# Kernel tuning notes

Measured on AMD Instinct MI355X. Metric: run time of the kernel, lower is better.

The kernel has to match this reference:

```python
import jax, jax.numpy as jnp
from jax import lax
import numpy as np

B, CIN, CP, H, W = 16, 64, 64, 64, 64
K1 = 3   # deformable kernel
K2 = 5   # parallel conv kernel
EPS = 1e-5


def conv2d(x, w, stride, pad):
    return lax.conv_general_dilated(
        x, w, (stride, stride), [(pad, pad), (pad, pad)],
        dimension_numbers=('NCHW', 'OIHW', 'NCHW'))


def batchnorm(x, g, b, m, v):
    scale = g / jnp.sqrt(v + EPS)
    return (x - m[None, :, None, None]) * scale[None, :, None, None] + b[None, :, None, None]


def deform_conv2d(x, offset, weight, stride, pad):
    # x: [B,Cin,H,W], offset: [B,2*K*K,Ho,Wo] (dy,dx interleaved per kernel tap, torchvision layout)
    Bn, Cin, Hn, Wn = x.shape
    Cout, _, K, _ = weight.shape
    KK = K * K
    Ho, Wo = offset.shape[2], offset.shape[3]
    off = offset.reshape(Bn, KK, 2, Ho, Wo)
    dy, dx = off[:, :, 0], off[:, :, 1]                      # [B,KK,Ho,Wo]
    ky, kx = jnp.meshgrid(jnp.arange(K), jnp.arange(K), indexing='ij')
    ky = ky.reshape(KK).astype(x.dtype)
    kx = kx.reshape(KK).astype(x.dtype)
    base_y = (jnp.arange(Ho) * stride - pad).astype(x.dtype)
    base_x = (jnp.arange(Wo) * stride - pad).astype(x.dtype)
    ys = base_y[None, None, :, None] + ky[None, :, None, None] + dy  # [B,KK,Ho,Wo]
    xs = base_x[None, None, None, :] + kx[None, :, None, None] + dx
    y0 = jnp.floor(ys); x0 = jnp.floor(xs)
    wy1 = ys - y0; wx1 = xs - x0
    wy0 = 1.0 - wy1; wx0 = 1.0 - wx1
    flat = x.reshape(Bn, Cin, Hn * Wn)

    def gather(yi, xi):
        valid = ((yi >= 0) & (yi <= Hn - 1) & (xi >= 0) & (xi <= Wn - 1))
        yc = jnp.clip(yi, 0, Hn - 1).astype(jnp.int32)
        xc = jnp.clip(xi, 0, Wn - 1).astype(jnp.int32)
        idx = (yc * Wn + xc).reshape(Bn, -1)                 # [B,KK*Ho*Wo]
        g = jax.vmap(lambda f, i: jnp.take(f, i, axis=1))(flat, idx)
        g = g.reshape(Bn, Cin, KK, Ho, Wo)
        return g * valid.astype(x.dtype)[:, None]

    val = (gather(y0, x0) * (wy0 * wx0)[:, None]
           + gather(y0, x0 + 1) * (wy0 * wx1)[:, None]
           + gather(y0 + 1, x0) * (wy1 * wx0)[:, None]
           + gather(y0 + 1, x0 + 1) * (wy1 * wx1)[:, None])   # [B,Cin,KK,Ho,Wo]
    w_r = weight.reshape(Cout, Cin, KK)
    return jnp.einsum('bcknm,ock->bonm', val, w_r)


def setup_inputs():
    key = jax.random.key(0)
    ks = jax.random.split(key, 18)
    f32 = jnp.float32
    x = jax.random.normal(ks[0], (B, CIN, H, W), f32)
    w_off = jax.random.normal(ks[1], (2 * K1 * K1, CIN, 3, 3), f32) * 0.01
    b_off = jnp.zeros((2 * K1 * K1,), f32)
    w1 = jax.random.normal(ks[2], (CP, CIN, K1, K1), f32) / np.sqrt(CIN * K1 * K1)
    w3 = jax.random.normal(ks[3], (CP, CIN, K2, K2), f32) / np.sqrt(CIN * K2 * K2)
    w2 = jax.random.normal(ks[4], (CP, CP, 3, 3), f32) / np.sqrt(CP * 9)
    def bn(i):
        g = jax.random.uniform(ks[5 + 4 * i], (CP,), f32, 0.5, 1.5)
        b = jax.random.normal(ks[6 + 4 * i], (CP,), f32) * 0.1
        m = jax.random.normal(ks[7 + 4 * i], (CP,), f32) * 0.1
        v = jax.random.uniform(ks[8 + 4 * i], (CP,), f32, 0.5, 1.5)
        return g, b, m, v
    g1, b1, m1, v1 = bn(0)
    g3, b3, m3, v3 = bn(1)
    g2, b2, m2, v2 = bn(2)
    return dict(x=x, w_off=w_off, b_off=b_off, w1=w1, g1=g1, b1=b1, m1=m1, v1=v1,
                w3=w3, g3=g3, b3=b3, m3=m3, v3=v3, w2=w2, g2=g2, b2=b2, m2=m2, v2=v2)


def reference(x, w_off, b_off, w1, g1, b1, m1, v1, w3, g3, b3, m3, v3, w2, g2, b2, m2, v2):
    offset1 = conv2d(x, w_off, 1, 1) + b_off[None, :, None, None]
    out = jax.nn.relu(batchnorm(deform_conv2d(x, offset1, w1, 1, 1), g1, b1, m1, v1))
    out_1 = jax.nn.relu(batchnorm(conv2d(x, w3, 1, 2), g3, b3, m3, v3))
    out = out + out_1
    out = batchnorm(conv2d(out, w2, 1, 1), g2, b2, m2, v2)
    out = out + x  # identity shortcut (stride=1, in_planes==planes)
    return jax.nn.relu(out)
```

## Files before the change

kernel.cpp:

```cpp
#include <hip/hip_runtime.h>
#include <hip/hip_bf16.h>


#define HWv 4096
#define EPSv 1e-5f

typedef __attribute__((ext_vector_type(8))) short bf16x8;
typedef __attribute__((ext_vector_type(16))) float f32x16;
typedef __attribute__((ext_vector_type(2))) float f32x2;

__device__ inline ushort f2bf(float f) {
  __hip_bfloat16 h = __float2bfloat16(f);
  return *(ushort*)&h;
}
__device__ inline float bitsf(unsigned int u) {
  union { unsigned int i; float f; } c; c.i = u; return c.f;
}

__global__ __launch_bounds__(256) void prep_kernel(
    const float* __restrict__ x, const float* __restrict__ w3,
    const float* __restrict__ w2, const float* __restrict__ w1,
    const float* __restrict__ w_off,
    ushort* __restrict__ xT, ushort* __restrict__ w3F,
    ushort* __restrict__ w2F, ushort* __restrict__ w1F,
    ushort* __restrict__ wofF) {
  __shared__ float tile[64][65];
  const int blk = blockIdx.x;
  if (blk < 1024) {
    const int y = blk & 63, b = blk >> 6;
    for (int i = threadIdx.x; i < 4096; i += 256) {
      int ci = i >> 6, xx = i & 63;
      tile[ci][xx] = x[(((size_t)b * 64 + ci) * 64 + y) * 64 + xx];
    }
    __syncthreads();
    for (int i = threadIdx.x; i < 2048; i += 256) {
      int xx = i >> 5, cip = (i & 31) * 2;
      ushort2 v;
      v.x = f2bf(tile[cip][xx]);
      v.y = f2bf(tile[cip + 1][xx]);
      *(ushort2*)&xT[(((size_t)b * 64 + y) * 64 + xx) * 64 + cip] = v;
    }
    return;
  }
  int idx = (blk - 1024) * 256 + threadIdx.x;
  if (idx < 102400) {
    int j = idx & 7, lane = (idx >> 3) & 63, ks = (idx >> 9) & 3;
    int half = (idx >> 11) & 1, kk = idx >> 12;
    int ln = lane & 31, kh = lane >> 5;
    int co = half * 32 + ln, ci = ks * 16 + kh * 8 + j;
    w3F[idx] = f2bf(w3[(co * 64 + ci) * 25 + kk]);
    return;
  }
  idx -= 102400;
  if (idx < 36864) {
    int j = idx & 7, lane = (idx >> 3) & 63, ks = (idx >> 9) & 3;
    int half = (idx >> 11) & 1, kk = idx >> 12;
    int ln = lane & 31, kh = lane >> 5;
    int co = half * 32 + ln, ci = ks * 16 + kh * 8 + j;
    w2F[idx] = f2bf(w2[(co * 64 + ci) * 9 + kk]);
    return;
  }
  idx -= 36864;
  if (idx < 36864) {
    int j = idx & 7, lane = (idx >> 3) & 63, ks = (idx >> 9) & 3;
    int half = (idx >> 11) & 1, kk = idx >> 12;
    int ln = lane & 31, kh = lane >> 5;
    int co = half * 32 + ln, ci = ks * 16 + kh * 8 + j;
    w1F[idx] = f2bf(w1[(co * 64 + ci) * 9 + kk]);
    return;
  }
  idx -= 36864;
  if (idx < 18432) {
    int j = idx & 7, lane = (idx >> 3) & 63, ks = (idx >> 9) & 3;
    int kk = idx >> 11;
    int ln = lane & 31, kh = lane >> 5;
    int ci = ks * 16 + kh * 8 + j;
    wofF[idx] = f2bf(ln < 18 ? w_off[(ln * 64 + ci) * 9 + kk] : 0.f);
  }
}

__device__ __forceinline__ bf16x8 blend4(bf16x8 va, bf16x8 vb, bf16x8 vc, bf16x8 vd,
                                         f32x2 w00v, f32x2 w01v, f32x2 w10v, f32x2 w11v) {
  const unsigned int* ua = (const unsigned int*)&va;
  const unsigned int* ub = (const unsigned int*)&vb;
  const unsigned int* uc = (const unsigned int*)&vc;
  const unsigned int* ud = (const unsigned int*)&vd;
  bf16x8 f;
  ushort2* fo = (ushort2*)&f;
#pragma unroll
  for (int d = 0; d < 4; ++d) {
    f32x2 av = {bitsf(ua[d] << 16), bitsf(ua[d] & 0xFFFF0000u)};
    f32x2 bv = {bitsf(ub[d] << 16), bitsf(ub[d] & 0xFFFF0000u)};
    f32x2 cv = {bitsf(uc[d] << 16), bitsf(uc[d] & 0xFFFF0000u)};
    f32x2 dv = {bitsf(ud[d] << 16), bitsf(ud[d] & 0xFFFF0000u)};
    f32x2 r = w00v * av + w01v * bv + w10v * cv + w11v * dv;
    __hip_bfloat162 h2 = __float22bfloat162_rn(make_float2(r.x, r.y));
    fo[d] = *(ushort2*)&h2;
  }
  return f;
}

__global__ __launch_bounds__(512, 4) void fused_kernel(
    const ushort* __restrict__ xT, const ushort* __restrict__ wofF,
    const float* __restrict__ b_off, const ushort* __restrict__ w1F,
    const ushort* __restrict__ w3F,
    const float* __restrict__ g1, const float* __restrict__ b1,
    const float* __restrict__ m1, const float* __restrict__ v1,
    const float* __restrict__ g3, const float* __restrict__ b3,
    const float* __restrict__ m3, const float* __restrict__ v3,
    ushort* __restrict__ s1T) {
  __shared__ __align__(16) unsigned char smem[71680];
  uint4* ldsx = (uint4*)smem;
  float* stash = (float*)(smem + 52224);
  float* bn1s = (float*)(smem + 70656);
  float* bn1b = bn1s + 64;
  float* bn3s = bn1s + 128;
  float* bn3b = bn1s + 192;

  const int tid = threadIdx.x;
  const int wv = tid >> 6, lane = tid & 63;
  const int ln = lane & 31, kh = lane >> 5;
  const int role = wv & 1, nt = (wv >> 1) & 1, r = wv >> 2;
  const int y0 = blockIdx.x * 2, b = blockIdx.y;
  const int y = y0 + r, px = nt * 32 + ln;
  const uint4* xT4 = (const uint4*)xT;
  const bool interior = (y0 >= 2 && y0 <= 60);

  if (tid < 64) {
    float s = g1[tid] * rsqrtf(v1[tid] + EPSv);
    bn1s[tid] = s; bn1b[tid] = b1[tid] - m1[tid] * s;
    float s3 = g3[tid] * rsqrtf(v3[tid] + EPSv);
    bn3s[tid] = s3; bn3b[tid] = b3[tid] - m3[tid] * s3;
  }
  for (int i = tid; i < 6 * 68 * 8; i += 512) {
    int tr = i / (68 * 8), rem = i % (68 * 8);
    int col = rem >> 3, c = rem & 7;
    int ysrc = min(max(y0 - 2 + tr, 0), 63);
    int xcol = col - 2;
    uint4 v = make_uint4(0, 0, 0, 0);
    if (xcol >= 0 && xcol <= 63)
      v = xT4[((size_t)((b * 64 + ysrc) * 64 + xcol)) * 8 + c];
    ldsx[(tr * 68 + col) * 8 + (c ^ (col & 7))] = v;
  }
  __syncthreads();

  {
    f32x16 acco;
#pragma unroll
    for (int j = 0; j < 16; ++j) acco[j] = 0.f;
    if (interior) {
#pragma unroll
      for (int kk = 0; kk < 9; ++kk) {
        const int ky = kk / 3, kx = kk % 3;
        const int tr = r + ky + 1;
        const int col = px + kx + 1;
#pragma unroll
        for (int ksq = 0; ksq < 2; ++ksq) {
          int ks = role * 2 + ksq;
          int c = ks * 2 + kh;
          bf16x8 af = *(const bf16x8*)&wofF[(size_t)((kk * 4 + ks) * 64 + lane) * 8];
          bf16x8 bf = *(const bf16x8*)&ldsx[(tr * 68 + col) * 8 + (c ^ (col & 7))];
          acco = __builtin_amdgcn_mfma_f32_32x32x16_bf16(af, bf, acco, 0, 0, 0);
        }
      }
    } else {
#pragma unroll
      for (int kk = 0; kk < 9; ++kk) {
        const int ky = kk / 3, kx = kk % 3;
        const int yy = y - 1 + ky;
        if (yy >= 0 && yy <= 63) {
          const int tr = yy - (y0 - 2);
          const int col = px + kx + 1;
#pragma unroll
          for (int ksq = 0; ksq < 2; ++ksq) {
            int ks = role * 2 + ksq;
            int c = ks * 2 + kh;
            bf16x8 af = *(const bf16x8*)&wofF[(size_t)((kk * 4 + ks) * 64 + lane) * 8];
            bf16x8 bf = *(const bf16x8*)&ldsx[(tr * 68 + col) * 8 + (c ^ (col & 7))];
            acco = __builtin_amdgcn_mfma_f32_32x32x16_bf16(af, bf, acco, 0, 0, 0);
          }
        }
      }
    }
    float* stb = stash + role * 2304;
#pragma unroll
    for (int reg = 0; reg < 16; ++reg) {
      int co = (reg & 3) + 8 * (reg >> 2) + 4 * kh;
      if (co < 18)
        stb[(r * 64 + px) * 18 + co] = acco[reg] + (role ? 0.f : b_off[co]);
    }
  }
  __syncthreads();

  f32x16 accA, accB;
#pragma unroll
  for (int j = 0; j < 16; ++j) { accA[j] = 0.f; accB[j] = 0.f; }

  if (role == 0) {
    float dyv[9], dxv[9];
    const int sb = (r * 64 + px) * 18;
#pragma unroll
    for (int kk = 0; kk < 9; ++kk) {
      dyv[kk] = stash[sb + 2 * kk] + stash[2304 + sb + 2 * kk];
      dxv[kk] = stash[sb + 2 * kk + 1] + stash[2304 + sb + 2 * kk + 1];
    }
    bool fast = true;
#pragma unroll
    for (int kk = 0; kk < 9; ++kk) {
      int iy0 = (int)floorf((float)(y - 1 + kk / 3) + dyv[kk]);
      int iy1 = iy0 + 1;
      bool ok0 = (iy0 < 0) || (iy0 > 63) || (iy0 >= y0 - 2 && iy0 <= y0 + 3);
      bool ok1 = (iy1 < 0) || (iy1 > 63) || (iy1 >= y0 - 2 && iy1 <= y0 + 3);
      fast = fast && ok0 && ok1;
    }
    const ushort* xb = xT + (size_t)b * 64 * 64 * 64;

    if (__ballot(!fast) == 0ull) {
#pragma unroll
      for (int kk = 0; kk < 9; ++kk) {
        const int ky = kk / 3, kx = kk % 3;
        float ys = (float)(y - 1 + ky) + dyv[kk];
        float xs = (float)(px - 1 + kx) + dxv[kk];
        float y0f = floorf(ys), x0f = floorf(xs);
        float wy1 = ys - y0f, wx1 = xs - x0f;
        float wy0 = 1.f - wy1, wx0 = 1.f - wx1;
        int iy0 = (int)y0f, ix0 = (int)x0f;
        int iy1 = iy0 + 1, ix1 = ix0 + 1;
        float vy0 = (iy0 >= 0 && iy0 <= 63) ? 1.f : 0.f;
        float vy1 = (iy1 >= 0 && iy1 <= 63) ? 1.f : 0.f;
        float vx0 = (ix0 >= 0 && ix0 <= 63) ? 1.f : 0.f;
        float vx1 = (ix1 >= 0 && ix1 <= 63) ? 1.f : 0.f;
        int x0c = min(max(ix0, 0), 63), x1c = min(max(ix1, 0), 63);
        float w00 = wy0 * wx0 * vy0 * vx0;
        float w01 = wy0 * wx1 * vy0 * vx1;
        float w10 = wy1 * wx0 * vy1 * vx0;
        float w11 = wy1 * wx1 * vy1 * vx1;
        int tr0 = min(max(iy0 - (y0 - 2), 0), 5);
        int tr1 = min(max(iy1 - (y0 - 2), 0), 5);
        int c0 = x0c + 2, c1 = x1c + 2;
        f32x2 w00v = {w00, w00}, w01v = {w01, w01};
        f32x2 w10v = {w10, w10}, w11v = {w11, w11};
#pragma unroll
        for (int ks = 0; ks < 4; ++ks) {
          int c = ks * 2 + kh;
          bf16x8 va = *(const bf16x8*)&ldsx[(tr0 * 68 + c0) * 8 + (c ^ (c0 & 7))];
          bf16x8 vb = *(const bf16x8*)&ldsx[(tr0 * 68 + c1) * 8 + (c ^ (c1 & 7))];
          bf16x8 vc = *(const bf16x8*)&ldsx[(tr1 * 68 + c0) * 8 + (c ^ (c0 & 7))];
          bf16x8 vd = *(const bf16x8*)&ldsx[(tr1 * 68 + c1) * 8 + (c ^ (c1 & 7))];
          bf16x8 f = blend4(va, vb, vc, vd, w00v, w01v, w10v, w11v);
          bf16x8 a0 = *(const bf16x8*)&w1F[(size_t)(((kk * 2 + 0) * 4 + ks) * 64 + lane) * 8];
          bf16x8 a1 = *(const bf16x8*)&w1F[(size_t)(((kk * 2 + 1) * 4 + ks) * 64 + lane) * 8];
          accA = __builtin_amdgcn_mfma_f32_32x32x16_bf16(a0, f, accA, 0, 0, 0);
          accB = __builtin_amdgcn_mfma_f32_32x32x16_bf16(a1, f, accB, 0, 0, 0);
        }
      }
    } else {
#pragma unroll
      for (int kk = 0; kk < 9; ++kk) {
        const int ky = kk / 3, kx = kk % 3;
        float ys = (float)(y - 1 + ky) + dyv[kk];
        float xs = (float)(px - 1 + kx) + dxv[kk];
        float y0f = floorf(ys), x0f = floorf(xs);
        float wy1 = ys - y0f, wx1 = xs - x0f;
        float wy0 = 1.f - wy1, wx0 = 1.f - wx1;
        int iy0 = (int)y0f, ix0 = (int)x0f;
        int iy1 = iy0 + 1, ix1 = ix0 + 1;
        float vy0 = (iy0 >= 0 && iy0 <= 63) ? 1.f : 0.f;
        float vy1 = (iy1 >= 0 && iy1 <= 63) ? 1.f : 0.f;
        float vx0 = (ix0 >= 0 && ix0 <= 63) ? 1.f : 0.f;
        float vx1 = (ix1 >= 0 && ix1 <= 63) ? 1.f : 0.f;
        int x0c = min(max(ix0, 0), 63), x1c = min(max(ix1, 0), 63);
        float w00 = wy0 * wx0 * vy0 * vx0;
        float w01 = wy0 * wx1 * vy0 * vx1;
        float w10 = wy1 * wx0 * vy1 * vx0;
        float w11 = wy1 * wx1 * vy1 * vx1;
        int tr0 = min(max(iy0 - (y0 - 2), 0), 5);
        int tr1 = min(max(iy1 - (y0 - 2), 0), 5);
        int c0 = x0c + 2, c1 = x1c + 2;
        f32x2 w00v = {w00, w00}, w01v = {w01, w01};
        f32x2 w10v = {w10, w10}, w11v = {w11, w11};
        int y0c = min(max(iy0, 0), 63), y1c = min(max(iy1, 0), 63);
        const ushort* p00 = xb + (y0c * 64 + x0c) * 64 + kh * 8;
        const ushort* p01 = xb + (y0c * 64 + x1c) * 64 + kh * 8;
        const ushort* p10 = xb + (y1c * 64 + x0c) * 64 + kh * 8;
        const ushort* p11 = xb + (y1c * 64 + x1c) * 64 + kh * 8;
#pragma unroll
        for (int ks = 0; ks < 4; ++ks) {
          int c = ks * 2 + kh;
          bf16x8 va = *(const bf16x8*)&ldsx[(tr0 * 68 + c0) * 8 + (c ^ (c0 & 7))];
          bf16x8 vb = *(const bf16x8*)&ldsx[(tr0 * 68 + c1) * 8 + (c ^ (c1 & 7))];
          bf16x8 vc = *(const bf16x8*)&ldsx[(tr1 * 68 + c0) * 8 + (c ^ (c0 & 7))];
          bf16x8 vd = *(const bf16x8*)&ldsx[(tr1 * 68 + c1) * 8 + (c ^ (c1 & 7))];
          bf16x8 f = blend4(va, vb, vc, vd, w00v, w01v, w10v, w11v);
          if (!fast) {
            bf16x8 ga = *(const bf16x8*)(p00 + ks * 16);
            bf16x8 gb = *(const bf16x8*)(p01 + ks * 16);
            bf16x8 gc = *(const bf16x8*)(p10 + ks * 16);
            bf16x8 gd = *(const bf16x8*)(p11 + ks * 16);
            f = blend4(ga, gb, gc, gd, w00v, w01v, w10v, w11v);
          }
          bf16x8 a0 = *(const bf16x8*)&w1F[(size_t)(((kk * 2 + 0) * 4 + ks) * 64 + lane) * 8];
          bf16x8 a1 = *(const bf16x8*)&w1F[(size_t)(((kk * 2 + 1) * 4 + ks) * 64 + lane) * 8];
          accA = __builtin_amdgcn_mfma_f32_32x32x16_bf16(a0, f, accA, 0, 0, 0);
          accB = __builtin_amdgcn_mfma_f32_32x32x16_bf16(a1, f, accB, 0, 0, 0);
        }
      }
    }
  } else {
    if (interior) {
#pragma unroll
      for (int kk = 0; kk < 25; ++kk) {
        const int ky = kk / 5, kx = kk % 5;
        const int tr = r + ky;
        const int col = px + kx;
        bf16x8 a0[4], a1[4], bfv[4];
#pragma unroll
        for (int ks = 0; ks < 4; ++ks) {
          a0[ks] = *(const bf16x8*)&w3F[(size_t)(((kk * 2 + 0) * 4 + ks) * 64 + lane) * 8];
          a1[ks] = *(const bf16x8*)&w3F[(size_t)(((kk * 2 + 1) * 4 + ks) * 64 + lane) * 8];
        }
#pragma unroll
        for (int ks = 0; ks < 4; ++ks) {
          int c = ks * 2 + kh;
          bfv[ks] = *(const bf16x8*)&ldsx[(tr * 68 + col) * 8 + (c ^ (col & 7))];
        }
#pragma unroll
        for (int ks = 0; ks < 4; ++ks) {
          accA = __builtin_amdgcn_mfma_f32_32x32x16_bf16(a0[ks], bfv[ks], accA, 0, 0, 0);
          accB = __builtin_amdgcn_mfma_f32_32x32x16_bf16(a1[ks], bfv[ks], accB, 0, 0, 0);
        }
      }
    } else {
#pragma unroll
      for (int kk = 0; kk < 25; ++kk) {
        const int ky = kk / 5, kx = kk % 5;
        const int yy = y - 2 + ky;
        if (yy >= 0 && yy <= 63) {
          const int tr = r + ky;
          const int col = px + kx;
#pragma unroll
          for (int ks = 0; ks < 4; ++ks) {
            int c = ks * 2 + kh;
            bf16x8 bf = *(const bf16x8*)&ldsx[(tr * 68 + col) * 8 + (c ^ (col & 7))];
            bf16x8 a0 = *(const bf16x8*)&w3F[(size_t)(((kk * 2 + 0) * 4 + ks) * 64 + lane) * 8];
            bf16x8 a1 = *(const bf16x8*)&w3F[(size_t)(((kk * 2 + 1) * 4 + ks) * 64 + lane) * 8];
            accA = __builtin_amdgcn_mfma_f32_32x32x16_bf16(a0, bf, accA, 0, 0, 0);
            accB = __builtin_amdgcn_mfma_f32_32x32x16_bf16(a1, bf, accB, 0, 0, 0);
          }
        }
      }
    }
  }

  __syncthreads();
  float4* sp = (float4*)((float*)smem + ((size_t)((r * 2 + nt) * 64 + lane)) * 32);
  const int sw = lane & 7;
  if (role) {
    union { f32x16 v; float4 q[4]; } ua, ub;
    ua.v = accA; ub.v = accB;
    sp[0 ^ sw] = ua.q[0]; sp[1 ^ sw] = ua.q[1];
    sp[2 ^ sw] = ua.q[2]; sp[3 ^ sw] = ua.q[3];
    sp[4 ^ sw] = ub.q[0]; sp[5 ^ sw] = ub.q[1];
    sp[6 ^ sw] = ub.q[2]; sp[7 ^ sw] = ub.q[3];
  }
  __syncthreads();
  if (!role) {
    union { f32x16 v; float4 q[4]; } ua, ub;
    ua.q[0] = sp[0 ^ sw]; ua.q[1] = sp[1 ^ sw];
    ua.q[2] = sp[2 ^ sw]; ua.q[3] = sp[3 ^ sw];
    ub.q[0] = sp[4 ^ sw]; ub.q[1] = sp[5 ^ sw];
    ub.q[2] = sp[6 ^ sw]; ub.q[3] = sp[7 ^ sw];

    ushort* op = s1T + ((size_t)((b * 64 + y) * 64 + px)) * 64;
#pragma unroll
    for (int q = 0; q < 4; ++q) {
      int co0 = 8 * q + 4 * kh;
      float vv[4];
#pragma unroll
      for (int rr = 0; rr < 4; ++rr) {
        int co = co0 + rr;
        float vd = accA[q * 4 + rr] * bn1s[co] + bn1b[co];
        vd = vd > 0.f ? vd : 0.f;
        float v5 = ua.v[q * 4 + rr] * bn3s[co] + bn3b[co];
        v5 = v5 > 0.f ? v5 : 0.f;
        vv[rr] = vd + v5;
      }
      ushort4 st;
      st.x = f2bf(vv[0]); st.y = f2bf(vv[1]); st.z = f2bf(vv[2]); st.w = f2bf(vv[3]);
      *(ushort4*)(op + co0) = st;
#pragma unroll
      for (int rr = 0; rr < 4; ++rr) {
        int co = co0 + 32 + rr;
        float vd = accB[q * 4 + rr] * bn1s[co] + bn1b[co];
        vd = vd > 0.f ? vd : 0.f;
        float v5 = ub.v[q * 4 + rr] * bn3s[co] + bn3b[co];
        v5 = v5 > 0.f ? v5 : 0.f;
        vv[rr] = vd + v5;
      }
      st.x = f2bf(vv[0]); st.y = f2bf(vv[1]); st.z = f2bf(vv[2]); st.w = f2bf(vv[3]);
      *(ushort4*)(op + co0 + 32) = st;
    }
  }
}

__global__ __launch_bounds__(256, 2) void conv3_mfma_kernel(
    const ushort* __restrict__ s1T, const ushort* __restrict__ w2F,
    const float* __restrict__ g2, const float* __restrict__ b2,
    const float* __restrict__ m2, const float* __restrict__ v2,
    const float* __restrict__ x, float* __restrict__ out) {
  __shared__ __align__(16) uint4 Bt[3 * 66 * 8];
  __shared__ float sc[64], bi[64];
  const int tid = threadIdx.x;
  if (tid < 64) {
    float s = g2[tid] * rsqrtf(v2[tid] + EPSv);
    sc[tid] = s;
    bi[tid] = b2[tid] - m2[tid] * s;
  }
  const int y = blockIdx.x, b = blockIdx.y;
  const int wv = tid >> 6, lane = tid & 63;
  const int ln = lane & 31, kh = lane >> 5;
  const int mh = wv & 1, nt = wv >> 1;
  const int px = nt * 32 + ln;
  const uint4* s1T4 = (const uint4*)s1T;

  for (int i = tid; i < 3 * 66 * 8; i += 256) {
    int tr = i / (66 * 8), rem = i % (66 * 8);
    int col = rem >> 3, c = rem & 7;
    int yy = y - 1 + tr, xcol = col - 1;
    uint4 v = make_uint4(0, 0, 0, 0);
    if (yy >= 0 && yy <= 63 && xcol >= 0 && xcol <= 63)
      v = s1T4[((size_t)((b * 64 + yy) * 64 + xcol)) * 8 + c];
    Bt[(tr * 66 + col) * 8 + (c ^ (col & 7))] = v;
  }
  __syncthreads();

  f32x16 acc;
#pragma unroll
  for (int j = 0; j < 16; ++j) acc[j] = 0.f;

#pragma unroll
  for (int kk = 0; kk < 9; ++kk) {
    const int ky = kk / 3, kx = kk % 3;
    const int col = px + kx;
    bf16x8 af[4], bfr[4];
#pragma unroll
    for (int ccb = 0; ccb < 4; ++ccb)
      af[ccb] = *(const bf16x8*)&w2F[(size_t)(((kk * 2 + mh) * 4 + ccb) * 64 + lane) * 8];
#pragma unroll
    for (int ccb = 0; ccb < 4; ++ccb) {
      int c = ccb * 2 + kh;
      bfr[ccb] = *(const bf16x8*)&Bt[(ky * 66 + col) * 8 + (c ^ (col & 7))];
    }
#pragma unroll
    for (int ccb = 0; ccb < 4; ++ccb)
      acc = __builtin_amdgcn_mfma_f32_32x32x16_bf16(af[ccb], bfr[ccb], acc, 0, 0, 0);
  }
#pragma unroll
  for (int reg = 0; reg < 16; ++reg) {
    int co = (reg & 3) + 8 * (reg >> 2) + 4 * kh + mh * 32;
    size_t o = (((size_t)b * 64 + co) * 64 + y) * 64 + px;
    float v = acc[reg] * sc[co] + bi[co] + x[o];
    out[o] = v > 0.f ? v : 0.f;
  }
}

extern "C" void kernel_launch(void* const* d_in, const int* in_sizes, int n_in,
                              void* d_out, int out_size, void* d_ws, size_t ws_size,
                              hipStream_t stream) {
  const float* x     = (const float*)d_in[0];
  const float* w_off = (const float*)d_in[1];
  const float* b_off = (const float*)d_in[2];
  const float* w1    = (const float*)d_in[3];
  const float* g1    = (const float*)d_in[4];
  const float* b1    = (const float*)d_in[5];
  const float* m1    = (const float*)d_in[6];
  const float* v1    = (const float*)d_in[7];
  const float* w3    = (const float*)d_in[8];
  const float* g3    = (const float*)d_in[9];
  const float* b3    = (const float*)d_in[10];
  const float* m3    = (const float*)d_in[11];
  const float* v3    = (const float*)d_in[12];
  const float* w2    = (const float*)d_in[13];
  const float* g2    = (const float*)d_in[14];
  const float* b2    = (const float*)d_in[15];
  const float* m2    = (const float*)d_in[16];
  const float* v2    = (const float*)d_in[17];
  float* out = (float*)d_out;

  ushort* xT   = (ushort*)d_ws;
  ushort* s1T  = xT + (size_t)16 * 64 * HWv;
  ushort* w3F  = s1T + (size_t)16 * 64 * HWv;
  ushort* w2F  = w3F + 102400;
  ushort* w1F  = w2F + 36864;
  ushort* wofF = w1F + 36864;

  prep_kernel<<<dim3(1024 + 760), dim3(256), 0, stream>>>(x, w3, w2, w1, w_off,
                                                          xT, w3F, w2F, w1F, wofF);
  fused_kernel<<<dim3(32, 16), dim3(512), 0, stream>>>(xT, wofF, b_off, w1F, w3F,
                                                       g1, b1, m1, v1, g3, b3, m3, v3,
                                                       s1T);
  conv3_mfma_kernel<<<dim3(64, 16), dim3(256), 0, stream>>>(s1T, w2F, g2, b2, m2, v2,
                                                            x, out);
}
```

Baseline: 70.37 us.

## Process one output row per block and compute offsets only in deform waves

The fused kernel now handles one output row per 256-thread block instead of two rows per 512-thread block, doubling the grid and shrinking the LDS halo tile from 6 to 5 rows. The offset-conv is no longer split across both wave roles with a shared-memory reduction and an extra barrier. The deform waves compute the full offset conv themselves and read it back without a block sync. This frees LDS and removes a sync, at the cost of more halo reloading per output row and serialising the offset conv onto the deform waves, which makes the two roles less balanced.

```diff
diff --git a/kernel.cpp b/kernel.cpp
--- a/kernel.cpp
+++ b/kernel.cpp
@@ -100,7 +100,7 @@
   return f;
 }
 
-__global__ __launch_bounds__(512, 4) void fused_kernel(
+__global__ __launch_bounds__(256, 3) void fused_kernel(
     const ushort* __restrict__ xT, const ushort* __restrict__ wofF,
     const float* __restrict__ b_off, const ushort* __restrict__ w1F,
     const ushort* __restrict__ w3F,
@@ -109,10 +109,10 @@
     const float* __restrict__ g3, const float* __restrict__ b3,
     const float* __restrict__ m3, const float* __restrict__ v3,
     ushort* __restrict__ s1T) {
-  __shared__ __align__(16) unsigned char smem[71680];
+  __shared__ __align__(16) unsigned char smem[49152];
   uint4* ldsx = (uint4*)smem;
-  float* stash = (float*)(smem + 52224);
-  float* bn1s = (float*)(smem + 70656);
+  float* stash = (float*)(smem + 43520);
+  float* bn1s = (float*)(smem + 48128);
   float* bn1b = bn1s + 64;
   float* bn3s = bn1s + 128;
   float* bn3b = bn1s + 192;
@@ -120,11 +120,10 @@
   const int tid = threadIdx.x;
   const int wv = tid >> 6, lane = tid & 63;
   const int ln = lane & 31, kh = lane >> 5;
-  const int role = wv & 1, nt = (wv >> 1) & 1, r = wv >> 2;
-  const int y0 = blockIdx.x * 2, b = blockIdx.y;
-  const int y = y0 + r, px = nt * 32 + ln;
+  const int role = wv & 1, nt = wv >> 1;
+  const int y = blockIdx.x, b = blockIdx.y;
+  const int px = nt * 32 + ln;
   const uint4* xT4 = (const uint4*)xT;
-  const bool interior = (y0 >= 2 && y0 <= 60);
 
   if (tid < 64) {
     float s = g1[tid] * rsqrtf(v1[tid] + EPSv);
@@ -132,10 +131,10 @@
     float s3 = g3[tid] * rsqrtf(v3[tid] + EPSv);
     bn3s[tid] = s3; bn3b[tid] = b3[tid] - m3[tid] * s3;
   }
-  for (int i = tid; i < 6 * 68 * 8; i += 512) {
+  for (int i = tid; i < 5 * 68 * 8; i += 256) {
     int tr = i / (68 * 8), rem = i % (68 * 8);
     int col = rem >> 3, c = rem & 7;
-    int ysrc = min(max(y0 - 2 + tr, 0), 63);
+    int ysrc = min(max(y - 2 + tr, 0), 63);
     int xcol = col - 2;
     uint4 v = make_uint4(0, 0, 0, 0);
     if (xcol >= 0 && xcol <= 63)
@@ -144,73 +143,68 @@
   }
   __syncthreads();
 
-  {
-    f32x16 acco;
-#pragma unroll
-    for (int j = 0; j < 16; ++j) acco[j] = 0.f;
-    if (interior) {
-#pragma unroll
-      for (int kk = 0; kk < 9; ++kk) {
-        const int ky = kk / 3, kx = kk % 3;
-        const int tr = r + ky + 1;
-        const int col = px + kx + 1;
-#pragma unroll
-        for (int ksq = 0; ksq < 2; ++ksq) {
-          int ks = role * 2 + ksq;
-          int c = ks * 2 + kh;
-          bf16x8 af = *(const bf16x8*)&wofF[(size_t)((kk * 4 + ks) * 64 + lane) * 8];
-          bf16x8 bf = *(const bf16x8*)&ldsx[(tr * 68 + col) * 8 + (c ^ (col & 7))];
-          acco = __builtin_amdgcn_mfma_f32_32x32x16_bf16(af, bf, acco, 0, 0, 0);
-        }
-      }
-    } else {
-#pragma unroll
-      for (int kk = 0; kk < 9; ++kk) {
-        const int ky = kk / 3, kx = kk % 3;
-        const int yy = y - 1 + ky;
-        if (yy >= 0 && yy <= 63) {
-          const int tr = yy - (y0 - 2);
+  f32x16 accA, accB;
+#pragma unroll
+  for (int j = 0; j < 16; ++j) { accA[j] = 0.f; accB[j] = 0.f; }
+
+  if (role == 0) {
+    {
+      f32x16 acco;
+#pragma unroll
+      for (int j = 0; j < 16; ++j) acco[j] = 0.f;
+      if (y >= 1 && y <= 62) {
+#pragma unroll
+        for (int kk = 0; kk < 9; ++kk) {
+          const int ky = kk / 3, kx = kk % 3;
+          const int tr = ky + 1;
           const int col = px + kx + 1;
 #pragma unroll
-          for (int ksq = 0; ksq < 2; ++ksq) {
-            int ks = role * 2 + ksq;
+          for (int ks = 0; ks < 4; ++ks) {
             int c = ks * 2 + kh;
             bf16x8 af = *(const bf16x8*)&wofF[(size_t)((kk * 4 + ks) * 64 + lane) * 8];
             bf16x8 bf = *(const bf16x8*)&ldsx[(tr * 68 + col) * 8 + (c ^ (col & 7))];
             acco = __builtin_amdgcn_mfma_f32_32x32x16_bf16(af, bf, acco, 0, 0, 0);
           }
         }
-      }
-    }
-    float* stb = stash + role * 2304;
-#pragma unroll
-    for (int reg = 0; reg < 16; ++reg) {
-      int co = (reg & 3) + 8 * (reg >> 2) + 4 * kh;
-      if (co < 18)
-        stb[(r * 64 + px) * 18 + co] = acco[reg] + (role ? 0.f : b_off[co]);
-    }
-  }
-  __syncthreads();
-
-  f32x16 accA, accB;
-#pragma unroll
-  for (int j = 0; j < 16; ++j) { accA[j] = 0.f; accB[j] = 0.f; }
-
-  if (role == 0) {
+      } else {
+#pragma unroll
+        for (int kk = 0; kk < 9; ++kk) {
+          const int ky = kk / 3, kx = kk % 3;
+          const int yy = y - 1 + ky;
+          if (yy >= 0 && yy <= 63) {
+            const int tr = ky + 1;
+            const int col = px + kx + 1;
+#pragma unroll
+            for (int ks = 0; ks < 4; ++ks) {
+              int c = ks * 2 + kh;
+              bf16x8 af = *(const bf16x8*)&wofF[(size_t)((kk * 4 + ks) * 64 + lane) * 8];
+              bf16x8 bf = *(const bf16x8*)&ldsx[(tr * 68 + col) * 8 + (c ^ (col & 7))];
+              acco = __builtin_amdgcn_mfma_f32_32x32x16_bf16(af, bf, acco, 0, 0, 0);
+            }
+          }
+        }
+      }
+#pragma unroll
+      for (int reg = 0; reg < 16; ++reg) {
+        int co = (reg & 3) + 8 * (reg >> 2) + 4 * kh;
+        if (co < 18)
+          stash[px * 18 + co] = acco[reg] + b_off[co];
+      }
+    }
+    asm volatile("" ::: "memory");
     float dyv[9], dxv[9];
-    const int sb = (r * 64 + px) * 18;
 #pragma unroll
     for (int kk = 0; kk < 9; ++kk) {
-      dyv[kk] = stash[sb + 2 * kk] + stash[2304 + sb + 2 * kk];
-      dxv[kk] = stash[sb + 2 * kk + 1] + stash[2304 + sb + 2 * kk + 1];
+      dyv[kk] = stash[px * 18 + 2 * kk];
+      dxv[kk] = stash[px * 18 + 2 * kk + 1];
     }
     bool fast = true;
 #pragma unroll
     for (int kk = 0; kk < 9; ++kk) {
       int iy0 = (int)floorf((float)(y - 1 + kk / 3) + dyv[kk]);
       int iy1 = iy0 + 1;
-      bool ok0 = (iy0 < 0) || (iy0 > 63) || (iy0 >= y0 - 2 && iy0 <= y0 + 3);
-      bool ok1 = (iy1 < 0) || (iy1 > 63) || (iy1 >= y0 - 2 && iy1 <= y0 + 3);
+      bool ok0 = (iy0 < 0) || (iy0 > 63) || (iy0 >= y - 2 && iy0 <= y + 2);
+      bool ok1 = (iy1 < 0) || (iy1 > 63) || (iy1 >= y - 2 && iy1 <= y + 2);
       fast = fast && ok0 && ok1;
     }
     const ushort* xb = xT + (size_t)b * 64 * 64 * 64;
@@ -235,8 +229,8 @@
         float w01 = wy0 * wx1 * vy0 * vx1;
         float w10 = wy1 * wx0 * vy1 * vx0;
         float w11 = wy1 * wx1 * vy1 * vx1;
-        int tr0 = min(max(iy0 - (y0 - 2), 0), 5);
-        int tr1 = min(max(iy1 - (y0 - 2), 0), 5);
+        int tr0 = min(max(iy0 - (y - 2), 0), 4);
+        int tr1 = min(max(iy1 - (y - 2), 0), 4);
         int c0 = x0c + 2, c1 = x1c + 2;
         f32x2 w00v = {w00, w00}, w01v = {w01, w01};
         f32x2 w10v = {w10, w10}, w11v = {w11, w11};
@@ -274,8 +268,8 @@
         float w01 = wy0 * wx1 * vy0 * vx1;
         float w10 = wy1 * wx0 * vy1 * vx0;
         float w11 = wy1 * wx1 * vy1 * vx1;
-        int tr0 = min(max(iy0 - (y0 - 2), 0), 5);
-        int tr1 = min(max(iy1 - (y0 - 2), 0), 5);
+        int tr0 = min(max(iy0 - (y - 2), 0), 4);
+        int tr1 = min(max(iy1 - (y - 2), 0), 4);
         int c0 = x0c + 2, c1 = x1c + 2;
         f32x2 w00v = {w00, w00}, w01v = {w01, w01};
         f32x2 w10v = {w10, w10}, w11v = {w11, w11};
@@ -307,11 +301,11 @@
       }
     }
   } else {
-    if (interior) {
+    if (y >= 2 && y <= 61) {
 #pragma unroll
       for (int kk = 0; kk < 25; ++kk) {
         const int ky = kk / 5, kx = kk % 5;
-        const int tr = r + ky;
+        const int tr = ky;
         const int col = px + kx;
         bf16x8 a0[4], a1[4], bfv[4];
 #pragma unroll
@@ -336,7 +330,7 @@
         const int ky = kk / 5, kx = kk % 5;
         const int yy = y - 2 + ky;
         if (yy >= 0 && yy <= 63) {
-          const int tr = r + ky;
+          const int tr = ky;
           const int col = px + kx;
 #pragma unroll
           for (int ks = 0; ks < 4; ++ks) {
@@ -353,7 +347,7 @@
   }
 
   __syncthreads();
-  float4* sp = (float4*)((float*)smem + ((size_t)((r * 2 + nt) * 64 + lane)) * 32);
+  float4* sp = (float4*)((float*)smem + ((size_t)(nt * 64 + lane)) * 32);
   const int sw = lane & 7;
   if (role) {
     union { f32x16 v; float4 q[4]; } ua, ub;
@@ -496,7 +490,7 @@
 
   prep_kernel<<<dim3(1024 + 760), dim3(256), 0, stream>>>(x, w3, w2, w1, w_off,
                                                           xT, w3F, w2F, w1F, wofF);
-  fused_kernel<<<dim3(32, 16), dim3(512), 0, stream>>>(xT, wofF, b_off, w1F, w3F,
+  fused_kernel<<<dim3(64, 16), dim3(256), 0, stream>>>(xT, wofF, b_off, w1F, w3F,
                                                        g1, b1, m1, v1, g3, b3, m3, v3,
                                                        s1T);
   conv3_mfma_kernel<<<dim3(64, 16), dim3(256), 0, stream>>>(s1T, w2F, g2, b2, m2, v2,
```

New measurement: 104.5 us. 48.5% more time.
